# Kernel optimization log

Measured on AMD Instinct MI355X. Metric: run time of the kernel, lower is better.

Reference implementation:

```python
import jax, jax.numpy as jnp
import numpy as np

K = 9
SIGMA = 4.0
RADIUS = 16  # round(4*sigma)
IMAGE_SHAPE = (256, 256)


def _gaussian_kernel_1d():
    i = jnp.arange(2 * RADIUS + 1, dtype=jnp.float32) - RADIUS
    g = jnp.exp(-(i ** 2) / (2.0 * SIGMA ** 2))
    return g / jnp.sum(g)


def _gaussian_blur(x):
    # x: [b, H, W, 1]; separable Gaussian blur, reflect-101 borders (cv2 default)
    g = _gaussian_kernel_1d()
    xp = jnp.pad(x, ((0, 0), (RADIUS, RADIUS), (RADIUS, RADIUS), (0, 0)), mode='reflect')
    dn = ('NHWC', 'HWIO', 'NHWC')
    kv = g.reshape(2 * RADIUS + 1, 1, 1, 1)  # vertical pass
    kh = g.reshape(1, 2 * RADIUS + 1, 1, 1)  # horizontal pass
    y = jax.lax.conv_general_dilated(xp, kv, (1, 1), 'VALID', dimension_numbers=dn)
    y = jax.lax.conv_general_dilated(y, kh, (1, 1), 'VALID', dimension_numbers=dn)
    return y


def setup_inputs() -> dict:
    key = jax.random.key(0)
    k1, k2 = jax.random.split(key)
    inputs = jax.random.normal(k1, (8, 32, 32, 512), dtype=jnp.float32)
    feature_vector = jax.random.normal(k2, (16384, 512), dtype=jnp.float32)
    return {"inputs": inputs, "feature_vector": feature_vector}


def reference(inputs, feature_vector):
    b, h, w, c = inputs.shape
    feat = inputs.reshape(b * h * w, c)
    # pairwise euclidean distances: [b*h*w, N]
    d2 = (jnp.sum(feat ** 2, axis=-1, keepdims=True)
          + jnp.sum(feature_vector ** 2, axis=-1)[None, :]
          - 2.0 * feat @ feature_vector.T)
    dist = jnp.sqrt(jnp.maximum(d2, 0.0))
    # k smallest distances, ascending (equivalent to tf.sort(...)[..., :k])
    neg_topk, _ = jax.lax.top_k(-dist, K)
    score = -neg_topk  # [b*h*w, K], ascending
    mask = score[:, 0].reshape(b, h, w, 1)
    score = score.reshape(b, h * w, K)
    # patch with maximal nearest-neighbor distance
    idx = jnp.argmax(score[..., 0], axis=-1)  # [b]
    conf = jnp.take_along_axis(score, idx[:, None, None], axis=1)[:, 0, :]  # [b, K]
    exp_conf = jnp.exp(conf)
    weight = 1.0 - jnp.max(exp_conf, axis=-1) / jnp.sum(exp_conf, axis=-1)
    score_out = (jnp.max(score[..., 0], axis=-1) * weight)[:, None]  # [b, 1]
    mask = jax.image.resize(mask, (b, *IMAGE_SHAPE, 1), method='bilinear', antialias=False)
    mask = _gaussian_blur(mask)
    return score_out, mask
```

## Files before the change

### kernel.cpp

```cpp
#include <hip/hip_runtime.h>

typedef __attribute__((ext_vector_type(8))) short bf16x8;
typedef __attribute__((ext_vector_type(4))) float f32x4;

static constexpr int M = 8192;
static constexpr int N = 16384;
static constexpr int K = 512;
static constexpr int BM = 256;
static constexpr int BN = 256;
static constexpr int RBLK = M / BM;
static constexpr int CBLK = N / BN;
static constexpr int BMs = 128;
static constexpr int BKs = 64;
static constexpr int KCHUNKS_S = K / BKs;
static constexpr int NGROUPS_S = 8;
static constexpr int GROUP_N_S = N / NGROUPS_S;
static constexpr int NTILES_S = GROUP_N_S / 128;
static constexpr float F_INF = 3.0e38f;

__device__ __forceinline__ unsigned short f2bf(float f) {
    unsigned int u = __float_as_uint(f);
    return (unsigned short)((u + 0x7fffu + ((u >> 16) & 1u)) >> 16);
}

__device__ __forceinline__ void gl_lds16(const void* g, void* l) {
    __builtin_amdgcn_global_load_lds(
        (const __attribute__((address_space(1))) unsigned int*)g,
        (__attribute__((address_space(3))) unsigned int*)l, 16, 0, 0);
}

__global__ void k_prep(const float* __restrict__ Q, const float* __restrict__ F,
                       unsigned short* __restrict__ Qb, unsigned short* __restrict__ Fb,
                       float* __restrict__ qn, float* __restrict__ fn) {
    int wid = blockIdx.x * 4 + (threadIdx.x >> 6);
    int lane = threadIdx.x & 63;
    bool isQ = wid < M;
    const float* src = isQ ? (Q + (size_t)wid * K) : (F + (size_t)(wid - M) * K);
    unsigned short* dst = isQ ? (Qb + (size_t)wid * K) : (Fb + (size_t)(wid - M) * K);
    const float4* p = reinterpret_cast<const float4*>(src) + lane * 2;
    float4 a = p[0], b = p[1];
    float s = a.x*a.x + a.y*a.y + a.z*a.z + a.w*a.w
            + b.x*b.x + b.y*b.y + b.z*b.z + b.w*b.w;
    bf16x8 v;
    v[0]=(short)f2bf(a.x); v[1]=(short)f2bf(a.y); v[2]=(short)f2bf(a.z); v[3]=(short)f2bf(a.w);
    v[4]=(short)f2bf(b.x); v[5]=(short)f2bf(b.y); v[6]=(short)f2bf(b.z); v[7]=(short)f2bf(b.w);
    *reinterpret_cast<bf16x8*>(dst + lane * 8) = v;
    #pragma unroll
    for (int d = 1; d < 64; d <<= 1) s += __shfl_xor(s, d);
    if (lane == 0) { if (isQ) qn[wid] = s; else fn[wid - M] = s; }
}

__global__ void k_norms(const float* __restrict__ Q, const float* __restrict__ F,
                        float* __restrict__ qn, float* __restrict__ fn) {
    int wid = blockIdx.x * 4 + (threadIdx.x >> 6);
    int lane = threadIdx.x & 63;
    const float* src = (wid < M) ? (Q + (size_t)wid * K) : (F + (size_t)(wid - M) * K);
    const float4* p = reinterpret_cast<const float4*>(src) + lane * 2;
    float4 a = p[0], b = p[1];
    float s = a.x*a.x + a.y*a.y + a.z*a.z + a.w*a.w
            + b.x*b.x + b.y*b.y + b.z*b.z + b.w*b.w;
    #pragma unroll
    for (int d = 1; d < 64; d <<= 1) s += __shfl_xor(s, d);
    if (lane == 0) { if (wid < M) qn[wid] = s; else fn[wid - M] = s; }
}

__global__ __launch_bounds__(512, 1)
void k_mingemm9(const unsigned short* __restrict__ Qb, const unsigned short* __restrict__ Fb,
                const float* __restrict__ qn, const float* __restrict__ fn,
                float* __restrict__ pv, unsigned int* __restrict__ pi) {
    __shared__ unsigned short As[2][2][8192];
    __shared__ unsigned short Bs[2][2][8192];
    __shared__ float redv[256][4];
    __shared__ unsigned int redi[256][4];

    const int tid = threadIdx.x;
    const int lane = tid & 63;
    const int wave = tid >> 6;
    const int wr = wave >> 2;
    const int wc = wave & 3;
    const int l15 = lane & 15, l4 = lane >> 4, l7 = lane & 7;
    const int r3 = lane >> 3;
    const int g8 = (lane & 7) ^ r3;

    const int wg = blockIdx.x;
    const int x = wg & 7, q = wg >> 3;
    const int c_blk = x * 8 + (q & 7);
    const int r_blk = q >> 3;
    const int row0 = r_blk * BM;
    const int col0 = c_blk * BN;

#define STAGE_A(t, hh) do {                                                        \
    _Pragma("unroll")                                                              \
    for (int i = 0; i < 2; ++i)                                                    \
        gl_lds16(Qb + (size_t)(row0 + (hh)*128 + i*64 + wave*8 + r3) * K           \
                    + (t)*64 + g8*8,                                               \
                 &As[(t)&1][hh][(i*64 + wave*8) * 64]);                            \
} while (0)
#define STAGE_B(t, hh) do {                                                        \
    _Pragma("unroll")                                                              \
    for (int i = 0; i < 2; ++i)                                                    \
        gl_lds16(Fb + (size_t)(col0 + (hh)*128 + i*64 + wave*8 + r3) * K           \
                    + (t)*64 + g8*8,                                               \
                 &Bs[(t)&1][hh][(i*64 + wave*8) * 64]);                            \
} while (0)

    f32x4 acc[8][4];
    #pragma unroll
    for (int a = 0; a < 8; ++a)
        #pragma unroll
        for (int b = 0; b < 4; ++b) acc[a][b] = f32x4{0.f, 0.f, 0.f, 0.f};

    bf16x8 afr[4][2], bfr[4][2];

#define PHASE(t, s, STMT, VMN) do {                                                \
    if ((s) == 0) {                                                                \
        _Pragma("unroll")                                                          \
        for (int f = 0; f < 4; ++f)                                                \
            _Pragma("unroll")                                                      \
            for (int ks = 0; ks < 2; ++ks)                                         \
                afr[f][ks] = *reinterpret_cast<const bf16x8*>(                     \
                    &As[(t)&1][wr][(f*16 + l15)*64 + (((ks*4 + l4) ^ l7))*8]);     \
        _Pragma("unroll")                                                          \
        for (int f = 0; f < 2; ++f)                                                \
            _Pragma("unroll")                                                      \
            for (int ks = 0; ks < 2; ++ks)                                         \
                bfr[f][ks] = *reinterpret_cast<const bf16x8*>(                     \
                    &Bs[(t)&1][0][(wc*32 + f*16 + l15)*64 + (((ks*4 + l4) ^ l7))*8]); \
    } else if ((s) == 1) {                                                         \
        _Pragma("unroll")                                                          \
        for (int f = 0; f < 2; ++f)                                                \
            _Pragma("unroll")                                                      \
            for (int ks = 0; ks < 2; ++ks)                                         \
                bfr[2 + f][ks] = *reinterpret_cast<const bf16x8*>(                 \
                    &Bs[(t)&1][1][(wc*32 + f*16 + l15)*64 + (((ks*4 + l4) ^ l7))*8]); \
    } else if ((s) == 2) {                                                         \
        _Pragma("unroll")                                                          \
        for (int f = 0; f < 4; ++f)                                                \
            _Pragma("unroll")                                                      \
            for (int ks = 0; ks < 2; ++ks)                                         \
                afr[f][ks] = *reinterpret_cast<const bf16x8*>(                     \
                    &As[(t)&1][wr][((f+4)*16 + l15)*64 + (((ks*4 + l4) ^ l7))*8]); \
    }                                                                              \
    STMT;                                                                          \
    __builtin_amdgcn_s_setprio(1);                                                 \
    {                                                                              \
        const int AB = ((s) >= 2) ? 4 : 0;                                         \
        const int FJ = ((s) & 1) ? 2 : 0;                                          \
        _Pragma("unroll")                                                          \
        for (int f = 0; f < 4; ++f)                                                \
            _Pragma("unroll")                                                      \
            for (int j2 = 0; j2 < 2; ++j2)                                         \
                _Pragma("unroll")                                                  \
                for (int ks = 0; ks < 2; ++ks)                                     \
                    acc[AB + f][FJ + j2] = __builtin_amdgcn_mfma_f32_16x16x32_bf16(\
                        afr[f][ks], bfr[FJ + j2][ks], acc[AB + f][FJ + j2], 0,0,0);\
    }                                                                              \
    __builtin_amdgcn_s_setprio(0);                                                 \
    asm volatile("s_waitcnt vmcnt(" #VMN ")" ::: "memory");                        \
    __builtin_amdgcn_s_barrier();                                                  \
    __builtin_amdgcn_sched_barrier(0);                                             \
} while (0)

    STAGE_B(0, 0); STAGE_B(0, 1); STAGE_A(0, 0); STAGE_A(0, 1);
    STAGE_B(1, 0); STAGE_B(1, 1); STAGE_A(1, 0);
    asm volatile("s_waitcnt vmcnt(6)" ::: "memory");
    __builtin_amdgcn_s_barrier();
    __builtin_amdgcn_sched_barrier(0);

#define ITER(T)                                        \
    PHASE(T,     0, STAGE_A((T)+1, 1), 6);             \
    PHASE(T,     1, STAGE_B((T)+2, 0), 6);             \
    PHASE(T,     2, STAGE_B((T)+2, 1), 6);             \
    PHASE(T,     3, STAGE_A((T)+2, 0), 6);             \
    PHASE((T)+1, 0, STAGE_A((T)+2, 1), 6);             \
    PHASE((T)+1, 1, STAGE_B((T)+3, 0), 6);             \
    PHASE((T)+1, 2, STAGE_B((T)+3, 1), 6);             \
    PHASE((T)+1, 3, STAGE_A((T)+3, 0), 6);

    ITER(0)
    ITER(2)
    ITER(4)
    PHASE(6, 0, STAGE_A(7, 1), 6);
    PHASE(6, 1, (void)0, 6);
    PHASE(6, 2, (void)0, 6);
    PHASE(6, 3, (void)0, 0);
    PHASE(7, 0, (void)0, 0);
    PHASE(7, 1, (void)0, 0);
    PHASE(7, 2, (void)0, 0);
    PHASE(7, 3, (void)0, 0);
#undef ITER
#undef PHASE
#undef STAGE_A
#undef STAGE_B

    float fnv[4];
    int colg[4];
    #pragma unroll
    for (int fj = 0; fj < 4; ++fj) {
        colg[fj] = col0 + (fj < 2 ? wc*32 + fj*16 : 128 + wc*32 + (fj - 2)*16) + l15;
        fnv[fj] = fn[colg[fj]];
    }
    #pragma unroll
    for (int fi = 0; fi < 8; ++fi) {
        #pragma unroll
        for (int j = 0; j < 4; ++j) {
            int rloc = wr*128 + fi*16 + l4*4 + j;
            float qv = qn[row0 + rloc];
            float v = F_INF; unsigned int ix = 0;
            #pragma unroll
            for (int fj = 0; fj < 4; ++fj) {
                float d2 = qv + fnv[fj] - 2.0f * acc[fi][fj][j];
                if (d2 < v) { v = d2; ix = (unsigned int)colg[fj]; }
            }
            #pragma unroll
            for (int d = 1; d < 16; d <<= 1) {
                float ov = __shfl_xor(v, d);
                unsigned int oi = (unsigned int)__shfl_xor((int)ix, d);
                if (ov < v) { v = ov; ix = oi; }
            }
            if (l15 == 0) { redv[rloc][wc] = v; redi[rloc][wc] = ix; }
        }
    }
    __syncthreads();
    if (tid < BM) {
        float v = redv[tid][0]; unsigned int ix = redi[tid][0];
        #pragma unroll
        for (int w2 = 1; w2 < 4; ++w2) {
            float ov = redv[tid][w2];
            if (ov < v) { v = ov; ix = redi[tid][w2]; }
        }
        pv[(size_t)(row0 + tid) * CBLK + c_blk] = v;
        pi[(size_t)(row0 + tid) * CBLK + c_blk] = ix;
    }
}

__global__ __launch_bounds__(256, 2)
void k_mingemm_cast(const float* __restrict__ Q, const float* __restrict__ F,
                    const float* __restrict__ qn, const float* __restrict__ fn,
                    float* __restrict__ pv, unsigned int* __restrict__ pi) {
    __shared__ unsigned short As[BMs * BKs];
    __shared__ unsigned short Bs[BMs * BKs];
    __shared__ float qn_t[BMs];
    __shared__ float fn_t[BMs];

    const int tid = threadIdx.x;
    const int lane = tid & 63;
    const int wave = tid >> 6;
    const int wr = wave >> 1, wc = wave & 1;
    const int l15 = lane & 15, l4 = lane >> 4;

    const int row0 = blockIdx.x * BMs;
    const int gbase = blockIdx.y * GROUP_N_S;

    const int srow = tid >> 3;
    const int p8 = tid & 7;
    const int g8 = p8 ^ (srow & 7);
    const float* pA[4];
    const float* pB[4];
    int dstOff[4];
    #pragma unroll
    for (int i = 0; i < 4; ++i) {
        int r = i * 32 + srow;
        pA[i] = Q + (size_t)(row0 + r) * K + g8 * 8;
        pB[i] = F + (size_t)(gbase + r) * K + g8 * 8;
        dstOff[i] = r * BKs + p8 * 8;
    }

    float mval[4][4];
    unsigned int midx[4][4];
    float qnv[4][4];
    #pragma unroll
    for (int a = 0; a < 4; ++a)
        #pragma unroll
        for (int b = 0; b < 4; ++b) { mval[a][b] = F_INF; midx[a][b] = 0; qnv[a][b] = 0.f; }

    for (int nt = 0; nt < NTILES_S; ++nt) {
        f32x4 acc[4][4];
        #pragma unroll
        for (int a = 0; a < 4; ++a)
            #pragma unroll
            for (int b = 0; b < 4; ++b) acc[a][b] = f32x4{0.f, 0.f, 0.f, 0.f};

        for (int kc = 0; kc < KCHUNKS_S; ++kc) {
            __syncthreads();
            #pragma unroll
            for (int i = 0; i < 4; ++i) {
                const float4* sa = reinterpret_cast<const float4*>(pA[i] + kc * BKs);
                float4 xa = sa[0], ya = sa[1];
                const float4* sb = reinterpret_cast<const float4*>(pB[i] + nt * (128 * K) + kc * BKs);
                float4 xb = sb[0], yb = sb[1];
                bf16x8 va, vb;
                va[0]=(short)f2bf(xa.x); va[1]=(short)f2bf(xa.y); va[2]=(short)f2bf(xa.z); va[3]=(short)f2bf(xa.w);
                va[4]=(short)f2bf(ya.x); va[5]=(short)f2bf(ya.y); va[6]=(short)f2bf(ya.z); va[7]=(short)f2bf(ya.w);
                vb[0]=(short)f2bf(xb.x); vb[1]=(short)f2bf(xb.y); vb[2]=(short)f2bf(xb.z); vb[3]=(short)f2bf(xb.w);
                vb[4]=(short)f2bf(yb.x); vb[5]=(short)f2bf(yb.y); vb[6]=(short)f2bf(yb.z); vb[7]=(short)f2bf(yb.w);
                *reinterpret_cast<bf16x8*>(&As[dstOff[i]]) = va;
                *reinterpret_cast<bf16x8*>(&Bs[dstOff[i]]) = vb;
            }
            if (kc == 0) {
                if (nt == 0 && tid < BMs) qn_t[tid] = qn[row0 + tid];
                if (tid < 128) fn_t[tid] = fn[gbase + nt * 128 + tid];
            }
            __syncthreads();
            if (nt == 0 && kc == 0) {
                #pragma unroll
                for (int fi = 0; fi < 4; ++fi)
                    #pragma unroll
                    for (int j = 0; j < 4; ++j)
                        qnv[fi][j] = qn_t[wr*64 + fi*16 + l4*4 + j];
            }
            #pragma unroll
            for (int ks = 0; ks < 2; ++ks) {
                const int gidx = ks * 4 + l4;
                bf16x8 af[4], bfv[4];
                #pragma unroll
                for (int fi = 0; fi < 4; ++fi) {
                    int r = wr*64 + fi*16 + l15;
                    int pg = gidx ^ (r & 7);
                    af[fi] = *reinterpret_cast<const bf16x8*>(&As[r*BKs + pg*8]);
                }
                #pragma unroll
                for (int fj = 0; fj < 4; ++fj) {
                    int r = wc*64 + fj*16 + l15;
                    int pg = gidx ^ (r & 7);
                    bfv[fj] = *reinterpret_cast<const bf16x8*>(&Bs[r*BKs + pg*8]);
                }
                #pragma unroll
                for (int fi = 0; fi < 4; ++fi)
                    #pragma unroll
                    for (int fj = 0; fj < 4; ++fj)
                        acc[fi][fj] = __builtin_amdgcn_mfma_f32_16x16x32_bf16(
                            af[fi], bfv[fj], acc[fi][fj], 0, 0, 0);
            }
        }
        const int colb = gbase + nt * 128 + wc * 64;
        float fnv[4];
        #pragma unroll
        for (int fj = 0; fj < 4; ++fj) fnv[fj] = fn_t[wc*64 + fj*16 + l15];
        #pragma unroll
        for (int fi = 0; fi < 4; ++fi) {
            #pragma unroll
            for (int j = 0; j < 4; ++j) {
                float qv = qnv[fi][j];
                #pragma unroll
                for (int fj = 0; fj < 4; ++fj) {
                    float d2 = qv + fnv[fj] - 2.0f * acc[fi][fj][j];
                    if (d2 < mval[fi][j]) {
                        mval[fi][j] = d2;
                        midx[fi][j] = (unsigned int)(colb + fj*16 + l15);
                    }
                }
            }
        }
    }
    #pragma unroll
    for (int fi = 0; fi < 4; ++fi) {
        #pragma unroll
        for (int j = 0; j < 4; ++j) {
            float v = mval[fi][j];
            unsigned int ix = midx[fi][j];
            #pragma unroll
            for (int d = 1; d < 16; d <<= 1) {
                float ov = __shfl_xor(v, d);
                unsigned int oi = (unsigned int)__shfl_xor((int)ix, d);
                if (ov < v) { v = ov; ix = oi; }
            }
            if (l15 == 0) {
                int rg = row0 + wr*64 + fi*16 + l4*4 + j;
                int pidx = rg * 16 + blockIdx.y * 2 + wc;
                pv[pidx] = v;
                pi[pidx] = ix;
            }
        }
    }
}

__global__ void k_refine(const float* __restrict__ Q, const float* __restrict__ F,
                         const float* __restrict__ pv, const unsigned int* __restrict__ pi,
                         float* __restrict__ minD, int PS) {
    int row = blockIdx.x * 4 + (threadIdx.x >> 6);
    int lane = threadIdx.x & 63;
    float v = F_INF; unsigned int ix = 0;
    for (int t = lane; t < PS; t += 64) {
        float nv = pv[(size_t)row*PS + t];
        if (nv < v) { v = nv; ix = pi[(size_t)row*PS + t]; }
    }
    #pragma unroll
    for (int d = 1; d < 64; d <<= 1) {
        float ov = __shfl_xor(v, d);
        unsigned int oi = (unsigned int)__shfl_xor((int)ix, d);
        if (ov < v) { v = ov; ix = oi; }
    }
    const float4* q = reinterpret_cast<const float4*>(Q + (size_t)row * K) + lane*2;
    const float4* f = reinterpret_cast<const float4*>(F + (size_t)ix * K) + lane*2;
    float4 a0 = q[0], a1 = q[1], b0 = f[0], b1 = f[1];
    float s = 0.f, dx;
    dx = a0.x-b0.x; s += dx*dx;  dx = a0.y-b0.y; s += dx*dx;
    dx = a0.z-b0.z; s += dx*dx;  dx = a0.w-b0.w; s += dx*dx;
    dx = a1.x-b1.x; s += dx*dx;  dx = a1.y-b1.y; s += dx*dx;
    dx = a1.z-b1.z; s += dx*dx;  dx = a1.w-b1.w; s += dx*dx;
    #pragma unroll
    for (int d = 1; d < 64; d <<= 1) s += __shfl_xor(s, d);
    if (lane == 0) minD[row] = sqrtf(s);
}

__global__ void k_argmax(const float* __restrict__ minD, unsigned int* __restrict__ sel) {
    __shared__ float sv[256];
    __shared__ int si[256];
    int b = blockIdx.x, tid = threadIdx.x;
    float bv = -F_INF; int bi = 0;
    for (int p = tid; p < 1024; p += 256) {
        float v = minD[b*1024 + p];
        if (v > bv) { bv = v; bi = p; }
    }
    sv[tid] = bv; si[tid] = bi;
    __syncthreads();
    for (int s = 128; s > 0; s >>= 1) {
        if (tid < s) {
            if (sv[tid+s] > sv[tid] || (sv[tid+s] == sv[tid] && si[tid+s] < si[tid])) {
                sv[tid] = sv[tid+s]; si[tid] = si[tid+s];
            }
        }
        __syncthreads();
    }
    if (tid == 0) sel[b] = (unsigned int)(b*1024 + si[0]);
}

__global__ void k_dist8(const float* __restrict__ Q, const float* __restrict__ F,
                        const unsigned int* __restrict__ sel, float* __restrict__ d2all) {
    __shared__ float qs[8][512];
    int tid = threadIdx.x;
    int lane = tid & 63, wave = tid >> 6;
    for (int i = tid; i < 8*512; i += 256) {
        int b = i >> 9;
        qs[b][i & 511] = Q[(size_t)sel[b] * K + (i & 511)];
    }
    __syncthreads();
    int base = blockIdx.x * 128 + wave * 32;
    for (int r = 0; r < 32; ++r) {
        int row = base + r;
        const float4* fp = reinterpret_cast<const float4*>(F + (size_t)row * K) + lane*2;
        float4 f0 = fp[0], f1 = fp[1];
        float fv[8] = {f0.x,f0.y,f0.z,f0.w,f1.x,f1.y,f1.z,f1.w};
        float accb[8];
        #pragma unroll
        for (int b = 0; b < 8; ++b) {
            float s = 0.f;
            #pragma unroll
            for (int e = 0; e < 8; ++e) {
                float d = fv[e] - qs[b][lane*8 + e];
                s += d * d;
            }
            accb[b] = s;
        }
        #pragma unroll
        for (int d = 1; d < 64; d <<= 1)
            #pragma unroll
            for (int b = 0; b < 8; ++b) accb[b] += __shfl_xor(accb[b], d);
        if (lane == 0) {
            #pragma unroll
            for (int b = 0; b < 8; ++b) d2all[b * N + row] = accb[b];
        }
    }
}

__global__ void k_sel9(const float* __restrict__ d2all, float* __restrict__ out) {
    __shared__ float sv[256 * 10];
    int b = blockIdx.x, tid = threadIdx.x;
    float v[9];
    #pragma unroll
    for (int i = 0; i < 9; ++i) v[i] = F_INF;
    for (int i = tid; i < N; i += 256) {
        float x = d2all[b * N + i];
        #pragma unroll
        for (int s = 0; s < 9; ++s) {
            float lo = fminf(v[s], x), hi = fmaxf(v[s], x);
            v[s] = lo; x = hi;
        }
    }
    #pragma unroll
    for (int i = 0; i < 9; ++i) sv[tid*10 + i] = v[i];
    sv[tid*10 + 9] = F_INF;
    __syncthreads();
    for (int s = 128; s > 0; s >>= 1) {
        if (tid < s) {
            int ia = 1, ib = 1;
            float av = sv[tid*10], bv = sv[(tid+s)*10];
            float c[9];
            #pragma unroll
            for (int k = 0; k < 9; ++k) {
                bool ta = av <= bv;
                c[k] = ta ? av : bv;
                float na = sv[tid*10 + ia], nb = sv[(tid+s)*10 + ib];
                if (ta) { av = na; ++ia; } else { bv = nb; ++ib; }
            }
            #pragma unroll
            for (int k = 0; k < 9; ++k) sv[tid*10 + k] = c[k];
        }
        __syncthreads();
    }
    if (tid == 0) {
        float c[9];
        #pragma unroll
        for (int i = 0; i < 9; ++i) c[i] = sqrtf(fmaxf(sv[i], 0.f));
        float S = 0.f;
        #pragma unroll
        for (int i = 0; i < 9; ++i) S += expf(c[i] - c[8]);
        out[b] = c[0] * (1.f - 1.f / S);
    }
}

__global__ void k_top9(const float* __restrict__ Q, const float* __restrict__ F,
                       const unsigned int* __restrict__ sel, float* __restrict__ part9) {
    __shared__ float qs[512];
    __shared__ float dist[2048];
    __shared__ float rv[256];
    __shared__ int ri[256];
    int b = blockIdx.x >> 3, g = blockIdx.x & 7;
    int tid = threadIdx.x;
    unsigned int srow = sel[b];
    if (tid < 128)
        reinterpret_cast<float4*>(qs)[tid] =
            reinterpret_cast<const float4*>(Q + (size_t)srow * K)[tid];
    __syncthreads();
    #pragma unroll
    for (int e = 0; e < 8; ++e) {
        int fl = tid + 256*e;
        const float* fp = F + (size_t)(g*2048 + fl) * K;
        float s = 0.f;
        for (int k = 0; k < 512; k += 4) {
            float4 fv4 = *reinterpret_cast<const float4*>(fp + k);
            float d0 = qs[k]   - fv4.x;
            float d1 = qs[k+1] - fv4.y;
            float d2 = qs[k+2] - fv4.z;
            float d3 = qs[k+3] - fv4.w;
            s += d0*d0 + d1*d1 + d2*d2 + d3*d3;
        }
        dist[fl] = s;
    }
    __syncthreads();
    for (int it = 0; it < 9; ++it) {
        float lv = F_INF; int li = 0;
        #pragma unroll
        for (int e = 0; e < 8; ++e) {
            int idx = tid + 256*e;
            float v = dist[idx];
            if (v < lv) { lv = v; li = idx; }
        }
        rv[tid] = lv; ri[tid] = li;
        __syncthreads();
        for (int s = 128; s > 0; s >>= 1) {
            if (tid < s && rv[tid+s] < rv[tid]) { rv[tid] = rv[tid+s]; ri[tid] = ri[tid+s]; }
            __syncthreads();
        }
        if (tid == 0) {
            part9[(b*8+g)*9 + it] = rv[0];
            dist[ri[0]] = F_INF;
        }
        __syncthreads();
    }
}

__global__ void k_final(const float* __restrict__ part9, float* __restrict__ out) {
    int b = threadIdx.x;
    if (b >= 8) return;
    float arr[9];
    #pragma unroll
    for (int i = 0; i < 9; ++i) arr[i] = F_INF;
    for (int g = 0; g < 8; ++g)
        for (int i = 0; i < 9; ++i) {
            float v = part9[(b*8+g)*9 + i];
            #pragma unroll
            for (int s = 0; s < 9; ++s) {
                float lo = fminf(arr[s], v), hi = fmaxf(arr[s], v);
                arr[s] = lo; v = hi;
            }
        }
    float c[9];
    #pragma unroll
    for (int i = 0; i < 9; ++i) c[i] = sqrtf(fmaxf(arr[i], 0.f));
    float c8 = c[8], S = 0.f;
    #pragma unroll
    for (int i = 0; i < 9; ++i) S += expf(c[i] - c8);
    float w = 1.f - 1.f / S;
    out[b] = c[0] * w;
}

__global__ void k_wmat(float* __restrict__ W) {
    int idx = blockIdx.x * 256 + threadIdx.x;
    int o = idx >> 5, j = idx & 31;
    float gsum = 0.f;
    #pragma unroll
    for (int u = 0; u < 33; ++u) { float d = (float)(u - 16); gsum += expf(-d*d * (1.f/32.f)); }
    float acc = 0.f;
    for (int u = 0; u < 33; ++u) {
        float d = (float)(u - 16);
        float gu = expf(-d*d * (1.f/32.f));
        int y = o + u - 16;
        y = y < 0 ? -y : (y > 255 ? 510 - y : y);
        float xin = ((float)y + 0.5f) * 0.125f - 0.5f;
        float j0f = floorf(xin);
        int j0 = (int)j0f;
        float wfr = xin - j0f;
        float r;
        if (j0 < 0) r = (j == 0) ? 1.f : 0.f;
        else if (j0 >= 31) r = (j == 31) ? 1.f : 0.f;
        else r = (j == j0) ? (1.f - wfr) : ((j == j0 + 1) ? wfr : 0.f);
        acc += gu * r;
    }
    W[idx] = acc / gsum;
}

__global__ void k_mask(const float* __restrict__ minD, const float* __restrict__ W,
                       float* __restrict__ outm) {
    __shared__ float Ms[1024];
    __shared__ float Ws[8192];
    __shared__ float Ts[8192];
    int b = blockIdx.x, tid = threadIdx.x;
    for (int i = tid; i < 1024; i += 256) Ms[i] = minD[b*1024 + i];
    for (int i = tid; i < 8192; i += 256) Ws[i] = W[i];
    __syncthreads();
    {
        int o = tid;
        float wrow[32];
        #pragma unroll
        for (int i = 0; i < 32; ++i) wrow[i] = Ws[o*32 + i];
        for (int j = 0; j < 32; ++j) {
            float s = 0.f;
            #pragma unroll
            for (int i = 0; i < 32; ++i) s += wrow[i] * Ms[i*32 + j];
            Ts[o*32 + j] = s;
        }
    }
    __syncthreads();
    {
        int p = tid;
        float wp[32];
        #pragma unroll
        for (int j = 0; j < 32; ++j) wp[j] = Ws[p*32 + j];
        float* dst = outm + (size_t)b * 65536;
        for (int o = 0; o < 256; ++o) {
            float s = 0.f;
            #pragma unroll
            for (int j = 0; j < 32; ++j) s += Ts[o*32 + j] * wp[j];
            dst[o*256 + p] = s;
        }
    }
}

extern "C" void kernel_launch(void* const* d_in, const int* in_sizes, int n_in,
                              void* d_out, int out_size, void* d_ws, size_t ws_size,
                              hipStream_t stream) {
    const float* Q = (const float*)d_in[0];
    const float* F = (const float*)d_in[1];
    float* out = (float*)d_out;

    const size_t smallFloats = (size_t)8192*64*2 + 8192 + 8 + 576 + (size_t)8*N + 8192 + 16384 + 8192;
    const size_t REQ = smallFloats*4 + (size_t)M*K*2 + (size_t)N*K*2;
    const bool fast = ws_size >= REQ;

    float* ws = (float*)d_ws;
    float* pv = ws;
    unsigned int* pi = (unsigned int*)(pv + 8192*64);
    float* minD = (float*)(pi + 8192*64);
    unsigned int* sel = (unsigned int*)(minD + 8192);
    float* part9 = (float*)(sel + 8);
    float* d2all = part9 + 576;
    float* qn = d2all + (size_t)8*N;
    float* fn = qn + 8192;
    float* W  = fn + 16384;
    unsigned short* Qb = (unsigned short*)(W + 8192);
    unsigned short* Fb = Qb + (size_t)M*K;

    k_wmat <<<dim3(32), 256, 0, stream>>>(W);
    if (fast) {
        k_prep <<<dim3((M + N) / 4), 256, 0, stream>>>(Q, F, Qb, Fb, qn, fn);
        k_mingemm9<<<dim3(RBLK * CBLK), 512, 0, stream>>>(Qb, Fb, qn, fn, pv, pi);
        k_refine<<<dim3(M / 4), 256, 0, stream>>>(Q, F, pv, pi, minD, 64);
        k_argmax<<<dim3(8), 256, 0, stream>>>(minD, sel);
        k_dist8<<<dim3(N / 128), 256, 0, stream>>>(Q, F, sel, d2all);
        k_sel9 <<<dim3(8), 256, 0, stream>>>(d2all, out);
    } else {
        k_norms<<<dim3((M + N) / 4), 256, 0, stream>>>(Q, F, qn, fn);
        k_mingemm_cast<<<dim3(M / BMs, NGROUPS_S), 256, 0, stream>>>(Q, F, qn, fn, pv, pi);
        k_refine<<<dim3(M / 4), 256, 0, stream>>>(Q, F, pv, pi, minD, 16);
        k_argmax<<<dim3(8), 256, 0, stream>>>(minD, sel);
        k_top9 <<<dim3(64), 256, 0, stream>>>(Q, F, sel, part9);
        k_final<<<dim3(1), 64, 0, stream>>>(part9, out);
    }
    k_mask <<<dim3(8), 256, 0, stream>>>(minD, W, out + 8);
}
```

Baseline: 335.1 us.

## Fuse argmax into refine via packed atomicMax, drop setprio and tile swizzle

The refine kernel now publishes each row's distance together with an inverted row index as a packed 64-bit value, and updates a per-batch slot with atomicMax. This removes the separate k_argmax launch on the fast path, and k_dist8 decodes the selected row directly. The packing keeps the lowest index on ties, matching argmax. The GEMM also switches from a grouped workgroup-to-tile mapping to a plain row-major mapping and drops the s_setprio hints around the MFMA block, which may change L2 reuse and wave scheduling.

```diff
diff --git a/kernel.cpp b/kernel.cpp
--- a/kernel.cpp
+++ b/kernel.cpp
@@ -83,9 +83,8 @@
     const int g8 = (lane & 7) ^ r3;
 
     const int wg = blockIdx.x;
-    const int x = wg & 7, q = wg >> 3;
-    const int c_blk = x * 8 + (q & 7);
-    const int r_blk = q >> 3;
+    const int c_blk = wg & 63;
+    const int r_blk = wg >> 6;
     const int row0 = r_blk * BM;
     const int col0 = c_blk * BN;
 
@@ -142,7 +141,6 @@
                     &As[(t)&1][wr][((f+4)*16 + l15)*64 + (((ks*4 + l4) ^ l7))*8]); \
     }                                                                              \
     STMT;                                                                          \
-    __builtin_amdgcn_s_setprio(1);                                                 \
     {                                                                              \
         const int AB = ((s) >= 2) ? 4 : 0;                                         \
         const int FJ = ((s) & 1) ? 2 : 0;                                          \
@@ -155,7 +153,6 @@
                     acc[AB + f][FJ + j2] = __builtin_amdgcn_mfma_f32_16x16x32_bf16(\
                         afr[f][ks], bfr[FJ + j2][ks], acc[AB + f][FJ + j2], 0,0,0);\
     }                                                                              \
-    __builtin_amdgcn_s_setprio(0);                                                 \
     asm volatile("s_waitcnt vmcnt(" #VMN ")" ::: "memory");                        \
     __builtin_amdgcn_s_barrier();                                                  \
     __builtin_amdgcn_sched_barrier(0);                                             \
@@ -377,7 +374,8 @@
 
 __global__ void k_refine(const float* __restrict__ Q, const float* __restrict__ F,
                          const float* __restrict__ pv, const unsigned int* __restrict__ pi,
-                         float* __restrict__ minD, int PS) {
+                         float* __restrict__ minD, unsigned long long* __restrict__ asel,
+                         int PS) {
     int row = blockIdx.x * 4 + (threadIdx.x >> 6);
     int lane = threadIdx.x & 63;
     float v = F_INF; unsigned int ix = 0;
@@ -401,7 +399,18 @@
     dx = a1.z-b1.z; s += dx*dx;  dx = a1.w-b1.w; s += dx*dx;
     #pragma unroll
     for (int d = 1; d < 64; d <<= 1) s += __shfl_xor(s, d);
-    if (lane == 0) minD[row] = sqrtf(s);
+    if (lane == 0) {
+        float dres = sqrtf(s);
+        minD[row] = dres;
+        unsigned long long pk =
+            ((unsigned long long)__float_as_uint(dres) << 32) |
+            (unsigned long long)(1023u - (unsigned int)(row & 1023));
+        atomicMax(asel + (row >> 10), pk);
+    }
+}
+
+__device__ __forceinline__ unsigned int sel_decode(unsigned long long pk, int b) {
+    return (unsigned int)(b * 1024 + (int)(1023u - (unsigned int)(pk & 0xffffffffu)));
 }
 
 __global__ void k_argmax(const float* __restrict__ minD, unsigned int* __restrict__ sel) {
@@ -427,13 +436,15 @@
 }
 
 __global__ void k_dist8(const float* __restrict__ Q, const float* __restrict__ F,
-                        const unsigned int* __restrict__ sel, float* __restrict__ d2all) {
+                        const unsigned long long* __restrict__ asel,
+                        float* __restrict__ d2all) {
     __shared__ float qs[8][512];
     int tid = threadIdx.x;
     int lane = tid & 63, wave = tid >> 6;
     for (int i = tid; i < 8*512; i += 256) {
         int b = i >> 9;
-        qs[b][i & 511] = Q[(size_t)sel[b] * K + (i & 511)];
+        unsigned int srow = sel_decode(asel[b], b);
+        qs[b][i & 511] = Q[(size_t)srow * K + (i & 511)];
     }
     __syncthreads();
     int base = blockIdx.x * 128 + wave * 32;
@@ -586,8 +597,9 @@
     out[b] = c[0] * w;
 }
 
-__global__ void k_wmat(float* __restrict__ W) {
+__global__ void k_wmat(float* __restrict__ W, unsigned long long* __restrict__ asel) {
     int idx = blockIdx.x * 256 + threadIdx.x;
+    if (idx < 8) asel[idx] = 0ull;
     int o = idx >> 5, j = idx & 31;
     float gsum = 0.f;
     #pragma unroll
@@ -655,7 +667,7 @@
     const float* F = (const float*)d_in[1];
     float* out = (float*)d_out;
 
-    const size_t smallFloats = (size_t)8192*64*2 + 8192 + 8 + 576 + (size_t)8*N + 8192 + 16384 + 8192;
+    const size_t smallFloats = (size_t)8192*64*2 + 8192 + 32 + 576 + (size_t)8*N + 8192 + 16384 + 8192;
     const size_t REQ = smallFloats*4 + (size_t)M*K*2 + (size_t)N*K*2;
     const bool fast = ws_size >= REQ;
 
@@ -663,7 +675,8 @@
     float* pv = ws;
     unsigned int* pi = (unsigned int*)(pv + 8192*64);
     float* minD = (float*)(pi + 8192*64);
-    unsigned int* sel = (unsigned int*)(minD + 8192);
+    unsigned long long* asel = (unsigned long long*)(minD + 8192);
+    unsigned int* sel = (unsigned int*)(asel + 8);
     float* part9 = (float*)(sel + 8);
     float* d2all = part9 + 576;
     float* qn = d2all + (size_t)8*N;
@@ -672,18 +685,17 @@
     unsigned short* Qb = (unsigned short*)(W + 8192);
     unsigned short* Fb = Qb + (size_t)M*K;
 
-    k_wmat <<<dim3(32), 256, 0, stream>>>(W);
+    k_wmat <<<dim3(32), 256, 0, stream>>>(W, asel);
     if (fast) {
         k_prep <<<dim3((M + N) / 4), 256, 0, stream>>>(Q, F, Qb, Fb, qn, fn);
         k_mingemm9<<<dim3(RBLK * CBLK), 512, 0, stream>>>(Qb, Fb, qn, fn, pv, pi);
-        k_refine<<<dim3(M / 4), 256, 0, stream>>>(Q, F, pv, pi, minD, 64);
-        k_argmax<<<dim3(8), 256, 0, stream>>>(minD, sel);
-        k_dist8<<<dim3(N / 128), 256, 0, stream>>>(Q, F, sel, d2all);
+        k_refine<<<dim3(M / 4), 256, 0, stream>>>(Q, F, pv, pi, minD, asel, 64);
+        k_dist8<<<dim3(N / 128), 256, 0, stream>>>(Q, F, asel, d2all);
         k_sel9 <<<dim3(8), 256, 0, stream>>>(d2all, out);
     } else {
         k_norms<<<dim3((M + N) / 4), 256, 0, stream>>>(Q, F, qn, fn);
         k_mingemm_cast<<<dim3(M / BMs, NGROUPS_S), 256, 0, stream>>>(Q, F, qn, fn, pv, pi);
-        k_refine<<<dim3(M / 4), 256, 0, stream>>>(Q, F, pv, pi, minD, 16);
+        k_refine<<<dim3(M / 4), 256, 0, stream>>>(Q, F, pv, pi, minD, asel, 16);
         k_argmax<<<dim3(8), 256, 0, stream>>>(minD, sel);
         k_top9 <<<dim3(64), 256, 0, stream>>>(Q, F, sel, part9);
         k_final<<<dim3(1), 64, 0, stream>>>(part9, out);
```

Measured after the change: 419.1 us. +25.1%, slower.
